# Kernel tuning notes

Hardware: AMD Instinct MI355X
Metric: run time of the kernel (lower is better)

The kernel has to match this reference:

```python
import jax, jax.numpy as jnp
import numpy as np

B, C, N, H = 2, 512, 3072, 8
D = C // H  # head_dim = 64


def setup_inputs() -> dict:
    key = jax.random.key(0)
    ks = jax.random.split(key, 8)
    s = 1.0 / np.sqrt(C)
    x = jax.random.normal(ks[0], (B, C, N), dtype=jnp.float32)
    adj = jax.random.randint(ks[1], (N, N), 0, 2, dtype=jnp.int32)
    adj = adj.at[jnp.arange(N), jnp.arange(N)].set(1)  # self-loops avoid empty rows
    geo_bias = jax.random.normal(ks[2], (N, N), dtype=jnp.float32) * 0.02
    Wq = jax.random.normal(ks[3], (C, C), dtype=jnp.float32) * s
    Wk = jax.random.normal(ks[4], (C, C), dtype=jnp.float32) * s
    Wv = jax.random.normal(ks[5], (C, C), dtype=jnp.float32) * s
    Wo = jax.random.normal(ks[6], (C, C), dtype=jnp.float32) * s
    z = jnp.zeros((C,), dtype=jnp.float32)
    return {"x": x, "adjacency": adj, "geo_bias": geo_bias,
            "Wq": Wq, "bq": z, "Wk": Wk, "bk": z, "Wv": Wv, "bv": z,
            "Wo": Wo, "bo": z}


def reference(x, adjacency, geo_bias, Wq, bq, Wk, bk, Wv, bv, Wo, bo):
    b, c, n = x.shape
    h, d = H, c // H
    feats = jnp.swapaxes(x, 1, 2)  # [B, N, C]
    # projections (nn.Linear: y = x @ W^T + b)
    q = feats @ Wq.T + bq
    k = feats @ Wk.T + bk
    v = feats @ Wv.T + bv
    # [B, H, N, D]
    q = q.reshape(b, n, h, d).transpose(0, 2, 1, 3)
    k = k.reshape(b, n, h, d).transpose(0, 2, 1, 3)
    v = v.reshape(b, n, h, d).transpose(0, 2, 1, 3)
    scores = jnp.einsum('bhnd,bhmd->bhnm', q, k) / jnp.sqrt(jnp.float32(d))
    scores = scores + geo_bias[None, None]
    scores = jnp.where(adjacency[None, None] == 0, -jnp.inf, scores)
    weights = jax.nn.softmax(scores, axis=-1)
    attended = jnp.einsum('bhnm,bhmd->bhnd', weights, v)
    attended = attended.transpose(0, 2, 1, 3).reshape(b, n, c)
    out = attended @ Wo.T + bo
    return jnp.swapaxes(out, 1, 2)  # [B, C, N]
```

## Files before the change

### kernel.cpp

```cpp
#include <hip/hip_runtime.h>

constexpr int Bb = 2, Cc = 512, Nn = 3072, Hh = 8, Dd = 64;
constexpr int BN = Bb * Nn;
constexpr int NT = Nn / 64;
constexpr int NTI = Nn / 128;

typedef __bf16 bf16;
typedef __attribute__((ext_vector_type(8))) __bf16 bf16x8;
typedef __attribute__((ext_vector_type(4))) __bf16 bf16x4;
typedef __attribute__((ext_vector_type(4))) float f32x4;
typedef __attribute__((ext_vector_type(16))) float f32x16;
typedef unsigned int u32;
typedef __attribute__((ext_vector_type(4))) u32 u32x4;

#define DEVINL static __device__ __forceinline__

DEVINL bf16x8 ldb8(const bf16* p) { return *reinterpret_cast<const bf16x8*>(p); }

DEVINL void gload_lds16(const bf16* g, bf16* l) {
    __builtin_amdgcn_global_load_lds(
        (const __attribute__((address_space(1))) void*)g,
        (__attribute__((address_space(3))) void*)l, 16, 0, 0);
}

DEVINL u32 cvtpk(float lo, float hi) {
    u32 r;
    asm("v_cvt_pk_bf16_f32 %0, %1, %2" : "=v"(r) : "v"(lo), "v"(hi));
    return r;
}
DEVINL void plswap(u32& a, u32& b) {
    asm("v_permlane32_swap_b32 %0, %1" : "+v"(a), "+v"(b));
}
DEVINL float xpair_sum(float v) { return v + __shfl_xor(v, 32); }

__global__ void k_tx(const float* __restrict__ x, bf16* __restrict__ feats) {
    __shared__ float t[32][33];
    const int b = blockIdx.z;
    const int n0 = blockIdx.x * 32, c0 = blockIdx.y * 32;
    const int tx = threadIdx.x, ty = threadIdx.y;
#pragma unroll
    for (int i = 0; i < 4; ++i)
        t[ty + i * 8][tx] = x[((size_t)b * Cc + c0 + ty + i * 8) * Nn + n0 + tx];
    __syncthreads();
#pragma unroll
    for (int i = 0; i < 4; ++i)
        feats[((size_t)b * Nn + n0 + ty + i * 8) * Cc + c0 + tx] = (bf16)t[tx][ty + i * 8];
}

__global__ void k_packw(const float* __restrict__ Wq, const float* __restrict__ Wk,
                        const float* __restrict__ Wv, const float* __restrict__ Wo,
                        bf16* __restrict__ Wqkv, bf16* __restrict__ WoB) {
    const int i = blockIdx.x * 256 + threadIdx.x;
    Wqkv[i]              = (bf16)Wq[i];
    Wqkv[i + 262144]     = (bf16)Wk[i];
    Wqkv[i + 524288]     = (bf16)Wv[i];
    WoB[i]               = (bf16)Wo[i];
}

__global__ void k_biasm(const int* __restrict__ adj, const float* __restrict__ gb,
                        bf16* __restrict__ biasF) {
    const int ti = blockIdx.x, tj = blockIdx.y;
    bf16* outp = biasF + ((size_t)ti * NT + tj) * 8192;
#pragma unroll
    for (int it = 0; it < 32; ++it) {
        const int p = it * 256 + threadIdx.x;
        const int w = p >> 11, hi = (p >> 10) & 1, l31 = (p >> 5) & 31;
        const int kt2 = (p >> 4) & 1, reg = p & 15;
        const int row = w * 32 + l31;
        const int col = kt2 * 32 + (reg & 3) + 8 * (reg >> 2) + 4 * hi;
        const size_t src = (size_t)(ti * 128 + row) * Nn + tj * 64 + col;
        outp[p] = adj[src] ? (bf16)(gb[src] * 1.44269504f) : (bf16)(-1e30f);
    }
}

#define STAGEG(dst, srcbase, ldk, k0, bi)                                      \
    {                                                                          \
        _Pragma("unroll")                                                      \
        for (int ps = 0; ps < 2; ++ps) {                                       \
            const int s = ps * 256 + tid;                                      \
            const int pr = s >> 3, pcb = s & 7;                                \
            const int cb = pcb ^ (pr & 7);                                     \
            gload_lds16((srcbase) + (size_t)pr * (ldk) + (k0) + cb * 8,        \
                        &dst[bi][(ps * 4 + w) * 512]);                         \
        }                                                                      \
    }

__global__ __launch_bounds__(256) void k_qkv(
        const bf16* __restrict__ feats, const bf16* __restrict__ Wqkv,
        const float* __restrict__ bq, const float* __restrict__ bk, const float* __restrict__ bv,
        bf16* __restrict__ Q, bf16* __restrict__ K, bf16* __restrict__ Vt) {
    __shared__ bf16 sA[2][4096];
    __shared__ bf16 sB[2][4096];
    const int m0 = blockIdx.x * 64;
    const int n0 = blockIdx.y * 64;
    const int tid = threadIdx.x, w = tid >> 6, lane = tid & 63;
    const int lg = lane >> 4, lc = lane & 15;

    f32x4 acc[4];
    const f32x4 z4 = {0.f, 0.f, 0.f, 0.f};
#pragma unroll
    for (int jt = 0; jt < 4; ++jt) acc[jt] = z4;

    const bf16* Abase = feats + (size_t)m0 * Cc;
    const bf16* Bbase = Wqkv + (size_t)n0 * Cc;

    int buf = 0;
    STAGEG(sA, Abase, Cc, 0, 0);
    STAGEG(sB, Bbase, Cc, 0, 0);
    for (int kk = 0; kk < 8; ++kk) {
        const int kn = (kk + 1 < 8) ? kk + 1 : 7;
        STAGEG(sA, Abase, Cc, kn * 64, buf ^ 1);
        STAGEG(sB, Bbase, Cc, kn * 64, buf ^ 1);
        asm volatile("s_waitcnt vmcnt(4)" ::: "memory");
        __builtin_amdgcn_s_barrier();
        const int ra = w * 16 + lc;
#pragma unroll
        for (int ks = 0; ks < 2; ++ks) {
            bf16x8 a = ldb8(&sA[buf][ra * 64 + (((ks * 4 + lg) ^ (ra & 7)) * 8)]);
#pragma unroll
            for (int jt = 0; jt < 4; ++jt) {
                const int rb = jt * 16 + lc;
                bf16x8 bfr = ldb8(&sB[buf][rb * 64 + (((ks * 4 + lg) ^ (rb & 7)) * 8)]);
                acc[jt] = __builtin_amdgcn_mfma_f32_16x16x32_bf16(a, bfr, acc[jt], 0, 0, 0);
            }
        }
        __builtin_amdgcn_s_barrier();
        buf ^= 1;
    }
    asm volatile("s_waitcnt vmcnt(0)" ::: "memory");

    const int proj = n0 >> 9;
    const int head = (n0 >> 6) & 7;
    const float* bias = proj == 0 ? bq : (proj == 1 ? bk : bv);
#pragma unroll
    for (int jt = 0; jt < 4; ++jt) {
        const int dcol = jt * 16 + lc;
        const float bs = bias[(n0 & 511) + dcol];
#pragma unroll
        for (int r = 0; r < 4; ++r) {
            const int m = m0 + w * 16 + lg * 4 + r;
            const int b = m / Nn;
            const int n = m - b * Nn;
            const float v = acc[jt][r] + bs;
            if (proj == 0)
                Q[(((size_t)b * Hh + head) * Nn + n) * Dd + dcol] = (bf16)v;
            else if (proj == 1)
                K[(((size_t)b * Hh + head) * Nn + n) * Dd + dcol] = (bf16)v;
            else
                Vt[(((size_t)b * Hh + head) * Dd + dcol) * Nn + n] = (bf16)v;
        }
    }
}

template <bool DIRECT, int TCNT>
__global__ __launch_bounds__(256) void k_attn(
        const bf16* __restrict__ Q, const bf16* __restrict__ K, const bf16* __restrict__ Vt,
        const bf16* __restrict__ biasF, bf16* __restrict__ att,
        float* __restrict__ pO, float* __restrict__ pL) {
    __shared__ bf16 sK[2][4096];
    __shared__ bf16 sV[2][4096];

    const int ti = blockIdx.x;
    const int i0 = ti * 128;
    const int bh = blockIdx.y;
    const int b = bh >> 3, h = bh & 7;
    const int sp = blockIdx.z;
    const int t0 = sp * TCNT;
    const int tid = threadIdx.x, w = tid >> 6, lane = tid & 63;
    const int l31 = lane & 31, hi = lane >> 5;

    const bf16* Qb = Q  + (size_t)bh * Nn * Dd;
    const bf16* Kb = K  + (size_t)bh * Nn * Dd;
    const bf16* Vb = Vt + (size_t)bh * Dd * Nn;
    const bf16* bp = biasF + (size_t)ti * NT * 8192 + (size_t)(w * 64 + lane) * 32;

    bf16x8 aq[4];
    {
        const bf16* qp = Qb + (size_t)(i0 + w * 32 + l31) * Dd + hi * 8;
#pragma unroll
        for (int dm = 0; dm < 4; ++dm) aq[dm] = ldb8(qp + dm * 16);
    }

    f32x16 acc[2];
#pragma unroll
    for (int dm = 0; dm < 2; ++dm)
#pragma unroll
        for (int i = 0; i < 16; ++i) acc[dm][i] = 0.f;
    float l16[16];
#pragma unroll
    for (int i = 0; i < 16; ++i) l16[i] = 0.f;

    constexpr float cqk = 0.18033688011112042f;

#define STAGE(bi, j0)                                                          \
    {                                                                          \
        _Pragma("unroll")                                                      \
        for (int u = 0; u < 2; ++u) {                                          \
            const int s = u * 256 + tid;                                       \
            const int pr = s >> 3, pcb = s & 7;                                \
            const int cb = pcb ^ (pr & 7);                                     \
            gload_lds16(Kb + (size_t)((j0) + pr) * Dd + cb * 8,                \
                        &sK[bi][(u * 4 + w) * 512]);                           \
            gload_lds16(Vb + (size_t)pr * Nn + (j0) + cb * 8,                  \
                        &sV[bi][(u * 4 + w) * 512]);                           \
        }                                                                      \
    }

    int buf = 0;
    STAGE(0, t0 * 64);
    bf16x8 bcur[4];
#pragma unroll
    for (int f = 0; f < 4; ++f) bcur[f] = ldb8(bp + (size_t)t0 * 8192 + f * 8);

    for (int u0 = 0; u0 < TCNT; ++u0) {
        const int tj = t0 + u0;
        const int tjn = (u0 + 1 < TCNT) ? tj + 1 : tj;
        STAGE(buf ^ 1, tjn * 64);
        bf16x8 bnx[4];
#pragma unroll
        for (int f = 0; f < 4; ++f) bnx[f] = ldb8(bp + (size_t)tjn * 8192 + f * 8);

        asm volatile("s_waitcnt vmcnt(8)" ::: "memory");
        __builtin_amdgcn_s_barrier();

        f32x16 s0, s1;
#pragma unroll
        for (int i = 0; i < 16; ++i) { s0[i] = 0.f; s1[i] = 0.f; }
        __builtin_amdgcn_s_setprio(1);
#pragma unroll
        for (int dm = 0; dm < 4; ++dm) {
            const int r0 = l31;
            bf16x8 kf0 = ldb8(&sK[buf][r0 * 64 + (((dm * 2 + hi) ^ (r0 & 7)) * 8)]);
            s0 = __builtin_amdgcn_mfma_f32_32x32x16_bf16(kf0, aq[dm], s0, 0, 0, 0);
            const int r1 = 32 + l31;
            bf16x8 kf1 = ldb8(&sK[buf][r1 * 64 + (((dm * 2 + hi) ^ (r1 & 7)) * 8)]);
            s1 = __builtin_amdgcn_mfma_f32_32x32x16_bf16(kf1, aq[dm], s1, 0, 0, 0);
        }
        __builtin_amdgcn_s_setprio(0);

        float sv[32];
#pragma unroll
        for (int i = 0; i < 16; ++i)
            sv[i] = __builtin_amdgcn_exp2f(__builtin_fmaf(s0[i], cqk, (float)bcur[i >> 3][i & 7]));
#pragma unroll
        for (int i = 0; i < 16; ++i)
            sv[16 + i] = __builtin_amdgcn_exp2f(__builtin_fmaf(s1[i], cqk, (float)bcur[2 + (i >> 3)][i & 7]));

#pragma unroll
        for (int i = 0; i < 16; ++i) l16[i] += sv[i] + sv[i + 16];

        bf16x8 pf[4];
#pragma unroll
        for (int g = 0; g < 4; ++g) {
            u32 X0 = cvtpk(sv[g * 8 + 0], sv[g * 8 + 1]);
            u32 X1 = cvtpk(sv[g * 8 + 2], sv[g * 8 + 3]);
            u32 Y0 = cvtpk(sv[g * 8 + 4], sv[g * 8 + 5]);
            u32 Y1 = cvtpk(sv[g * 8 + 6], sv[g * 8 + 7]);
            plswap(X0, Y0);
            plswap(X1, Y1);
            u32x4 t4 = {X0, X1, Y0, Y1};
            pf[g] = __builtin_bit_cast(bf16x8, t4);
        }

        __builtin_amdgcn_s_setprio(1);
#pragma unroll
        for (int dm = 0; dm < 2; ++dm)
#pragma unroll
            for (int kt = 0; kt < 4; ++kt) {
                const int rv = dm * 32 + l31;
                bf16x8 vf = ldb8(&sV[buf][rv * 64 + (((kt * 2 + hi) ^ (rv & 7)) * 8)]);
                acc[dm] = __builtin_amdgcn_mfma_f32_32x32x16_bf16(vf, pf[kt], acc[dm], 0, 0, 0);
            }
        __builtin_amdgcn_s_setprio(0);

        __builtin_amdgcn_s_barrier();
#pragma unroll
        for (int f = 0; f < 4; ++f) bcur[f] = bnx[f];
        buf ^= 1;
    }
    asm volatile("s_waitcnt vmcnt(0)" ::: "memory");

#pragma unroll
    for (int i = 0; i < 8; ++i) l16[i] += l16[i + 8];
#pragma unroll
    for (int i = 0; i < 4; ++i) l16[i] += l16[i + 4];
    float lrow = (l16[0] + l16[1]) + (l16[2] + l16[3]);
    lrow = xpair_sum(lrow);

    const int q = i0 + w * 32 + l31;
    if (DIRECT) {
        const float inv = 1.f / lrow;
        bf16* ap = att + ((size_t)b * Nn + q) * Cc + h * 64;
#pragma unroll
        for (int dm = 0; dm < 2; ++dm)
#pragma unroll
            for (int rg = 0; rg < 4; ++rg) {
                bf16x4 o;
#pragma unroll
                for (int i = 0; i < 4; ++i) o[i] = (bf16)(acc[dm][rg * 4 + i] * inv);
                *reinterpret_cast<bf16x4*>(ap + dm * 32 + rg * 8 + hi * 4) = o;
            }
    } else {
        float* op = pO + ((size_t)(sp * Bb * Hh + bh) * Nn + q) * Dd;
#pragma unroll
        for (int dm = 0; dm < 2; ++dm)
#pragma unroll
            for (int rg = 0; rg < 4; ++rg) {
                f32x4 o;
#pragma unroll
                for (int i = 0; i < 4; ++i) o[i] = acc[dm][rg * 4 + i];
                *reinterpret_cast<f32x4*>(op + dm * 32 + rg * 8 + hi * 4) = o;
            }
        if (hi == 0) pL[(size_t)(sp * Bb * Hh + bh) * Nn + q] = lrow;
    }
#undef STAGE
}

__global__ __launch_bounds__(256) void k_comb(const float* __restrict__ pO,
                                              const float* __restrict__ pL,
                                              bf16* __restrict__ att, int nsplit) {
    const int bh = blockIdx.y, b = bh >> 3, h = bh & 7;
    const int q = blockIdx.x * 64 + (threadIdx.x >> 2);
    const int d0 = (threadIdx.x & 3) * 16;
    const size_t base = ((size_t)bh * Nn + q) * Dd + d0;
    const size_t soff = (size_t)Bb * Hh * Nn * Dd;
    const size_t loff = (size_t)Bb * Hh * Nn;
    float l = 0.f;
    f32x4 o[4];
#pragma unroll
    for (int i = 0; i < 4; ++i) o[i] = f32x4{0.f, 0.f, 0.f, 0.f};
    for (int s = 0; s < nsplit; ++s) {
        l += pL[s * loff + (size_t)bh * Nn + q];
#pragma unroll
        for (int i = 0; i < 4; ++i) {
            f32x4 o2 = *reinterpret_cast<const f32x4*>(pO + s * soff + base + i * 4);
#pragma unroll
            for (int j = 0; j < 4; ++j) o[i][j] += o2[j];
        }
    }
    const float inv = 1.f / l;
    bf16* ap = att + ((size_t)b * Nn + q) * Cc + h * 64 + d0;
#pragma unroll
    for (int i = 0; i < 4; ++i) {
        bf16x4 ov;
#pragma unroll
        for (int j = 0; j < 4; ++j) ov[j] = (bf16)(o[i][j] * inv);
        *reinterpret_cast<bf16x4*>(ap + i * 4) = ov;
    }
}

__global__ __launch_bounds__(256) void k_out(
        const bf16* __restrict__ att, const bf16* __restrict__ WoB,
        const float* __restrict__ bo, float* __restrict__ out) {
    __shared__ bf16 sA[2][4096];
    __shared__ bf16 sB[2][4096];
    const int m0 = blockIdx.x * 64;
    const int n0 = blockIdx.y * 64;
    const int tid = threadIdx.x, w = tid >> 6, lane = tid & 63;
    const int lg = lane >> 4, lc = lane & 15;

    f32x4 acc[4];
    const f32x4 z4 = {0.f, 0.f, 0.f, 0.f};
#pragma unroll
    for (int jt = 0; jt < 4; ++jt) acc[jt] = z4;

    const bf16* Abase = att + (size_t)m0 * Cc;
    const bf16* Bbase = WoB + (size_t)n0 * Cc;

    int buf = 0;
    STAGEG(sA, Abase, Cc, 0, 0);
    STAGEG(sB, Bbase, Cc, 0, 0);
    for (int kk = 0; kk < 8; ++kk) {
        const int kn = (kk + 1 < 8) ? kk + 1 : 7;
        STAGEG(sA, Abase, Cc, kn * 64, buf ^ 1);
        STAGEG(sB, Bbase, Cc, kn * 64, buf ^ 1);
        asm volatile("s_waitcnt vmcnt(4)" ::: "memory");
        __builtin_amdgcn_s_barrier();
        const int ra = w * 16 + lc;
#pragma unroll
        for (int ks = 0; ks < 2; ++ks) {
            bf16x8 a = ldb8(&sA[buf][ra * 64 + (((ks * 4 + lg) ^ (ra & 7)) * 8)]);
#pragma unroll
            for (int jt = 0; jt < 4; ++jt) {
                const int rb = jt * 16 + lc;
                bf16x8 bfr = ldb8(&sB[buf][rb * 64 + (((ks * 4 + lg) ^ (rb & 7)) * 8)]);
                acc[jt] = __builtin_amdgcn_mfma_f32_16x16x32_bf16(a, bfr, acc[jt], 0, 0, 0);
            }
        }
        __builtin_amdgcn_s_barrier();
        buf ^= 1;
    }
    asm volatile("s_waitcnt vmcnt(0)" ::: "memory");

    const int m = m0 + w * 16 + lg * 4;
    const int b = m / Nn;
    const int n = m - b * Nn;
#pragma unroll
    for (int jt = 0; jt < 4; ++jt) {
        const int col = n0 + jt * 16 + lc;
        const float bs = bo[col];
        f32x4 vv;
#pragma unroll
        for (int r = 0; r < 4; ++r) vv[r] = acc[jt][r] + bs;
        *reinterpret_cast<f32x4*>(&out[((size_t)b * Cc + col) * Nn + n]) = vv;
    }
}

extern "C" void kernel_launch(void* const* d_in, const int* in_sizes, int n_in,
                              void* d_out, int out_size, void* d_ws, size_t ws_size,
                              hipStream_t stream) {
    (void)in_sizes; (void)n_in; (void)out_size;
    const float* x  = (const float*)d_in[0];
    const int*   adj= (const int*)d_in[1];
    const float* gb = (const float*)d_in[2];
    const float* Wq = (const float*)d_in[3];
    const float* bq = (const float*)d_in[4];
    const float* Wk = (const float*)d_in[5];
    const float* bk = (const float*)d_in[6];
    const float* Wv = (const float*)d_in[7];
    const float* bv = (const float*)d_in[8];
    const float* Wo = (const float*)d_in[9];
    const float* bo = (const float*)d_in[10];
    float* out = (float*)d_out;

    char* ws = (char*)d_ws;
    bf16*  feats = (bf16*)(ws);
    bf16*  Wqkv  = (bf16*)(ws + 6291456);
    bf16*  WoB   = (bf16*)(ws + 7864320);
    bf16*  Qm    = (bf16*)(ws + 8388608);
    bf16*  Km    = (bf16*)(ws + 14680064);
    bf16*  Vt    = (bf16*)(ws + 20971520);
    bf16*  att   = (bf16*)(ws + 27262976);
    bf16*  biasF = (bf16*)(ws + 33554432);
    float* pO    = (float*)(ws + 52428800);

    const size_t PO1 = 12582912ull, PL1 = 196608ull, BASE = 52428800ull;
    const size_t need4 = BASE + 4 * PO1 + 4 * PL1;
    const size_t need2 = BASE + 2 * PO1 + 2 * PL1;
    const size_t need1 = BASE + 1 * PO1 + 1 * PL1;

    k_tx   <<<dim3(Nn / 32, Cc / 32, Bb), dim3(32, 8), 0, stream>>>(x, feats);
    k_packw<<<dim3(1024), dim3(256), 0, stream>>>(Wq, Wk, Wv, Wo, Wqkv, WoB);
    k_biasm<<<dim3(NTI, NT), dim3(256), 0, stream>>>(adj, gb, biasF);
    k_qkv  <<<dim3(BN / 64, 1536 / 64), dim3(256), 0, stream>>>(feats, Wqkv, bq, bk, bv, Qm, Km, Vt);

    if (ws_size >= need4) {
        float* pL = (float*)(ws + BASE + 4 * PO1);
        k_attn<false, NT / 4><<<dim3(NTI, Bb * Hh, 4), dim3(256), 0, stream>>>(
            Qm, Km, Vt, biasF, att, pO, pL);
        k_comb<<<dim3(Nn / 64, Bb * Hh), dim3(256), 0, stream>>>(pO, pL, att, 4);
    } else if (ws_size >= need2) {
        float* pL = (float*)(ws + BASE + 2 * PO1);
        k_attn<false, NT / 2><<<dim3(NTI, Bb * Hh, 2), dim3(256), 0, stream>>>(
            Qm, Km, Vt, biasF, att, pO, pL);
        k_comb<<<dim3(Nn / 64, Bb * Hh), dim3(256), 0, stream>>>(pO, pL, att, 2);
    } else if (ws_size >= need1) {
        float* pL = (float*)(ws + BASE + 1 * PO1);
        k_attn<false, NT><<<dim3(NTI, Bb * Hh, 1), dim3(256), 0, stream>>>(
            Qm, Km, Vt, biasF, att, pO, pL);
        k_comb<<<dim3(Nn / 64, Bb * Hh), dim3(256), 0, stream>>>(pO, pL, att, 1);
    } else {
        k_attn<true, NT><<<dim3(NTI, Bb * Hh, 1), dim3(256), 0, stream>>>(
            Qm, Km, Vt, biasF, att, pO, (float*)pO);
    }
    k_out  <<<dim3(BN / 64, Cc / 64), dim3(256), 0, stream>>>(att, WoB, bo, out);
}
```

Measured before the change: 156.9 us.

## Enlarge projection GEMM tiles to 128x128 and drop 4-way attention split

The QKV and output projection GEMMs move from 64x64 to 128x128 block tiles, with each wave computing a 64x64 sub-tile of 4x4 MFMA fragments so every loaded A and B fragment is reused across more MFMAs. This cuts LDS and global traffic per FLOP but uses more registers and LDS, and launches fewer blocks (for example 48x4=192 blocks for k_out). Separately, the 4-way key-split attention path is removed, so attention now uses the 2-way split with a combine step, trading partial-sum traffic against parallelism.

```diff
diff --git a/kernel.cpp b/kernel.cpp
--- a/kernel.cpp
+++ b/kernel.cpp
@@ -73,15 +73,37 @@
     }
 }
 
-#define STAGEG(dst, srcbase, ldk, k0, bi)                                      \
+#define STAGE128(dst, srcbase, ldk, k0, bi)                                    \
     {                                                                          \
         _Pragma("unroll")                                                      \
-        for (int ps = 0; ps < 2; ++ps) {                                       \
-            const int s = ps * 256 + tid;                                      \
+        for (int uu = 0; uu < 4; ++uu) {                                       \
+            const int s = uu * 256 + tid;                                      \
             const int pr = s >> 3, pcb = s & 7;                                \
             const int cb = pcb ^ (pr & 7);                                     \
             gload_lds16((srcbase) + (size_t)pr * (ldk) + (k0) + cb * 8,        \
-                        &dst[bi][(ps * 4 + w) * 512]);                         \
+                        &dst[bi][(uu * 4 + w) * 512]);                         \
+        }                                                                      \
+    }
+
+#define GEMM128_STEP(bi)                                                       \
+    {                                                                          \
+        _Pragma("unroll")                                                      \
+        for (int ks = 0; ks < 2; ++ks) {                                       \
+            bf16x8 af[4];                                                      \
+            _Pragma("unroll")                                                  \
+            for (int rt = 0; rt < 4; ++rt) {                                   \
+                const int ra = wr * 64 + rt * 16 + lc;                         \
+                af[rt] = ldb8(&sA[bi][ra * 64 + (((ks * 4 + lg) ^ (ra & 7)) * 8)]); \
+            }                                                                  \
+            _Pragma("unroll")                                                  \
+            for (int ct = 0; ct < 4; ++ct) {                                   \
+                const int rb = wc * 64 + ct * 16 + lc;                         \
+                bf16x8 bfv = ldb8(&sB[bi][rb * 64 + (((ks * 4 + lg) ^ (rb & 7)) * 8)]); \
+                _Pragma("unroll")                                              \
+                for (int rt = 0; rt < 4; ++rt)                                 \
+                    acc[rt][ct] = __builtin_amdgcn_mfma_f32_16x16x32_bf16(     \
+                        af[rt], bfv, acc[rt][ct], 0, 0, 0);                    \
+            }                                                                  \
         }                                                                      \
     }
 
@@ -89,65 +111,61 @@
         const bf16* __restrict__ feats, const bf16* __restrict__ Wqkv,
         const float* __restrict__ bq, const float* __restrict__ bk, const float* __restrict__ bv,
         bf16* __restrict__ Q, bf16* __restrict__ K, bf16* __restrict__ Vt) {
-    __shared__ bf16 sA[2][4096];
-    __shared__ bf16 sB[2][4096];
-    const int m0 = blockIdx.x * 64;
-    const int n0 = blockIdx.y * 64;
+    __shared__ bf16 sA[2][8192];
+    __shared__ bf16 sB[2][8192];
+    const int m0 = blockIdx.x * 128;
+    const int n0 = blockIdx.y * 128;
     const int tid = threadIdx.x, w = tid >> 6, lane = tid & 63;
     const int lg = lane >> 4, lc = lane & 15;
-
-    f32x4 acc[4];
+    const int wr = w >> 1, wc = w & 1;
+
+    f32x4 acc[4][4];
     const f32x4 z4 = {0.f, 0.f, 0.f, 0.f};
 #pragma unroll
-    for (int jt = 0; jt < 4; ++jt) acc[jt] = z4;
+    for (int rt = 0; rt < 4; ++rt)
+#pragma unroll
+        for (int ct = 0; ct < 4; ++ct) acc[rt][ct] = z4;
 
     const bf16* Abase = feats + (size_t)m0 * Cc;
     const bf16* Bbase = Wqkv + (size_t)n0 * Cc;
 
     int buf = 0;
-    STAGEG(sA, Abase, Cc, 0, 0);
-    STAGEG(sB, Bbase, Cc, 0, 0);
+    STAGE128(sA, Abase, Cc, 0, 0);
+    STAGE128(sB, Bbase, Cc, 0, 0);
     for (int kk = 0; kk < 8; ++kk) {
         const int kn = (kk + 1 < 8) ? kk + 1 : 7;
-        STAGEG(sA, Abase, Cc, kn * 64, buf ^ 1);
-        STAGEG(sB, Bbase, Cc, kn * 64, buf ^ 1);
-        asm volatile("s_waitcnt vmcnt(4)" ::: "memory");
-        __builtin_amdgcn_s_barrier();
-        const int ra = w * 16 + lc;
-#pragma unroll
-        for (int ks = 0; ks < 2; ++ks) {
-            bf16x8 a = ldb8(&sA[buf][ra * 64 + (((ks * 4 + lg) ^ (ra & 7)) * 8)]);
-#pragma unroll
-            for (int jt = 0; jt < 4; ++jt) {
-                const int rb = jt * 16 + lc;
-                bf16x8 bfr = ldb8(&sB[buf][rb * 64 + (((ks * 4 + lg) ^ (rb & 7)) * 8)]);
-                acc[jt] = __builtin_amdgcn_mfma_f32_16x16x32_bf16(a, bfr, acc[jt], 0, 0, 0);
+        STAGE128(sA, Abase, Cc, kn * 64, buf ^ 1);
+        STAGE128(sB, Bbase, Cc, kn * 64, buf ^ 1);
+        asm volatile("s_waitcnt vmcnt(8)" ::: "memory");
+        __builtin_amdgcn_s_barrier();
+        GEMM128_STEP(buf);
+        __builtin_amdgcn_s_barrier();
+        buf ^= 1;
+    }
+    asm volatile("s_waitcnt vmcnt(0)" ::: "memory");
+
+    const int proj = n0 >> 9;
+    const int head = ((n0 & 511) >> 6) + wc;
+    const float* bias = proj == 0 ? bq : (proj == 1 ? bk : bv);
+#pragma unroll
+    for (int ct = 0; ct < 4; ++ct) {
+        const int d = ct * 16 + lc;
+        const float bs = bias[(n0 & 511) + wc * 64 + d];
+#pragma unroll
+        for (int rt = 0; rt < 4; ++rt) {
+#pragma unroll
+            for (int i = 0; i < 4; ++i) {
+                const int m = m0 + wr * 64 + rt * 16 + lg * 4 + i;
+                const int b = m / Nn;
+                const int n = m - b * Nn;
+                const float v = acc[rt][ct][i] + bs;
+                if (proj == 0)
+                    Q[(((size_t)b * Hh + head) * Nn + n) * Dd + d] = (bf16)v;
+                else if (proj == 1)
+                    K[(((size_t)b * Hh + head) * Nn + n) * Dd + d] = (bf16)v;
+                else
+                    Vt[(((size_t)b * Hh + head) * Dd + d) * Nn + n] = (bf16)v;
             }
-        }
-        __builtin_amdgcn_s_barrier();
-        buf ^= 1;
-    }
-    asm volatile("s_waitcnt vmcnt(0)" ::: "memory");
-
-    const int proj = n0 >> 9;
-    const int head = (n0 >> 6) & 7;
-    const float* bias = proj == 0 ? bq : (proj == 1 ? bk : bv);
-#pragma unroll
-    for (int jt = 0; jt < 4; ++jt) {
-        const int dcol = jt * 16 + lc;
-        const float bs = bias[(n0 & 511) + dcol];
-#pragma unroll
-        for (int r = 0; r < 4; ++r) {
-            const int m = m0 + w * 16 + lg * 4 + r;
-            const int b = m / Nn;
-            const int n = m - b * Nn;
-            const float v = acc[jt][r] + bs;
-            if (proj == 0)
-                Q[(((size_t)b * Hh + head) * Nn + n) * Dd + dcol] = (bf16)v;
-            else if (proj == 1)
-                K[(((size_t)b * Hh + head) * Nn + n) * Dd + dcol] = (bf16)v;
-            else
-                Vt[(((size_t)b * Hh + head) * Dd + dcol) * Nn + n] = (bf16)v;
         }
     }
 }
@@ -352,57 +370,53 @@
 __global__ __launch_bounds__(256) void k_out(
         const bf16* __restrict__ att, const bf16* __restrict__ WoB,
         const float* __restrict__ bo, float* __restrict__ out) {
-    __shared__ bf16 sA[2][4096];
-    __shared__ bf16 sB[2][4096];
-    const int m0 = blockIdx.x * 64;
-    const int n0 = blockIdx.y * 64;
+    __shared__ bf16 sA[2][8192];
+    __shared__ bf16 sB[2][8192];
+    const int m0 = blockIdx.x * 128;
+    const int n0 = blockIdx.y * 128;
     const int tid = threadIdx.x, w = tid >> 6, lane = tid & 63;
     const int lg = lane >> 4, lc = lane & 15;
-
-    f32x4 acc[4];
+    const int wr = w >> 1, wc = w & 1;
+
+    f32x4 acc[4][4];
     const f32x4 z4 = {0.f, 0.f, 0.f, 0.f};
 #pragma unroll
-    for (int jt = 0; jt < 4; ++jt) acc[jt] = z4;
+    for (int rt = 0; rt < 4; ++rt)
+#pragma unroll
+        for (int ct = 0; ct < 4; ++ct) acc[rt][ct] = z4;
 
     const bf16* Abase = att + (size_t)m0 * Cc;
     const bf16* Bbase = WoB + (size_t)n0 * Cc;
 
     int buf = 0;
-    STAGEG(sA, Abase, Cc, 0, 0);
-    STAGEG(sB, Bbase, Cc, 0, 0);
+    STAGE128(sA, Abase, Cc, 0, 0);
+    STAGE128(sB, Bbase, Cc, 0, 0);
     for (int kk = 0; kk < 8; ++kk) {
         const int kn = (kk + 1 < 8) ? kk + 1 : 7;
-        STAGEG(sA, Abase, Cc, kn * 64, buf ^ 1);
-        STAGEG(sB, Bbase, Cc, kn * 64, buf ^ 1);
-        asm volatile("s_waitcnt vmcnt(4)" ::: "memory");
-        __builtin_amdgcn_s_barrier();
-        const int ra = w * 16 + lc;
-#pragma unroll
-        for (int ks = 0; ks < 2; ++ks) {
-            bf16x8 a = ldb8(&sA[buf][ra * 64 + (((ks * 4 + lg) ^ (ra & 7)) * 8)]);
-#pragma unroll
-            for (int jt = 0; jt < 4; ++jt) {
-                const int rb = jt * 16 + lc;
-                bf16x8 bfr = ldb8(&sB[buf][rb * 64 + (((ks * 4 + lg) ^ (rb & 7)) * 8)]);
-                acc[jt] = __builtin_amdgcn_mfma_f32_16x16x32_bf16(a, bfr, acc[jt], 0, 0, 0);
-            }
+        STAGE128(sA, Abase, Cc, kn * 64, buf ^ 1);
+        STAGE128(sB, Bbase, Cc, kn * 64, buf ^ 1);
+        asm volatile("s_waitcnt vmcnt(8)" ::: "memory");
+        __builtin_amdgcn_s_barrier();
+        GEMM128_STEP(buf);
+        __builtin_amdgcn_s_barrier();
+        buf ^= 1;
+    }
+    asm volatile("s_waitcnt vmcnt(0)" ::: "memory");
+
+#pragma unroll
+    for (int ct = 0; ct < 4; ++ct) {
+        const int col = n0 + wc * 64 + ct * 16 + lc;
+        const float bs = bo[col];
+#pragma unroll
+        for (int rt = 0; rt < 4; ++rt) {
+            const int m = m0 + wr * 64 + rt * 16 + lg * 4;
+            const int b = m / Nn;
+            const int n = m - b * Nn;
+            f32x4 vv;
+#pragma unroll
+            for (int i = 0; i < 4; ++i) vv[i] = acc[rt][ct][i] + bs;
+            *reinterpret_cast<f32x4*>(&out[((size_t)b * Cc + col) * Nn + n]) = vv;
         }
-        __builtin_amdgcn_s_barrier();
-        buf ^= 1;
-    }
-    asm volatile("s_waitcnt vmcnt(0)" ::: "memory");
-
-    const int m = m0 + w * 16 + lg * 4;
-    const int b = m / Nn;
-    const int n = m - b * Nn;
-#pragma unroll
-    for (int jt = 0; jt < 4; ++jt) {
-        const int col = n0 + jt * 16 + lc;
-        const float bs = bo[col];
-        f32x4 vv;
-#pragma unroll
-        for (int r = 0; r < 4; ++r) vv[r] = acc[jt][r] + bs;
-        *reinterpret_cast<f32x4*>(&out[((size_t)b * Cc + col) * Nn + n]) = vv;
     }
 }
 
@@ -435,21 +449,15 @@
     float* pO    = (float*)(ws + 52428800);
 
     const size_t PO1 = 12582912ull, PL1 = 196608ull, BASE = 52428800ull;
-    const size_t need4 = BASE + 4 * PO1 + 4 * PL1;
     const size_t need2 = BASE + 2 * PO1 + 2 * PL1;
     const size_t need1 = BASE + 1 * PO1 + 1 * PL1;
 
     k_tx   <<<dim3(Nn / 32, Cc / 32, Bb), dim3(32, 8), 0, stream>>>(x, feats);
     k_packw<<<dim3(1024), dim3(256), 0, stream>>>(Wq, Wk, Wv, Wo, Wqkv, WoB);
     k_biasm<<<dim3(NTI, NT), dim3(256), 0, stream>>>(adj, gb, biasF);
-    k_qkv  <<<dim3(BN / 64, 1536 / 64), dim3(256), 0, stream>>>(feats, Wqkv, bq, bk, bv, Qm, Km, Vt);
-
-    if (ws_size >= need4) {
-        float* pL = (float*)(ws + BASE + 4 * PO1);
-        k_attn<false, NT / 4><<<dim3(NTI, Bb * Hh, 4), dim3(256), 0, stream>>>(
-            Qm, Km, Vt, biasF, att, pO, pL);
-        k_comb<<<dim3(Nn / 64, Bb * Hh), dim3(256), 0, stream>>>(pO, pL, att, 4);
-    } else if (ws_size >= need2) {
+    k_qkv  <<<dim3(BN / 128, 1536 / 128), dim3(256), 0, stream>>>(feats, Wqkv, bq, bk, bv, Qm, Km, Vt);
+
+    if (ws_size >= need2) {
         float* pL = (float*)(ws + BASE + 2 * PO1);
         k_attn<false, NT / 2><<<dim3(NTI, Bb * Hh, 2), dim3(256), 0, stream>>>(
             Qm, Km, Vt, biasF, att, pO, pL);
@@ -463,5 +471,5 @@
         k_attn<true, NT><<<dim3(NTI, Bb * Hh, 1), dim3(256), 0, stream>>>(
             Qm, Km, Vt, biasF, att, pO, (float*)pO);
     }
-    k_out  <<<dim3(BN / 64, Cc / 64), dim3(256), 0, stream>>>(att, WoB, bo, out);
-}
+    k_out  <<<dim3(BN / 128, Cc / 128), dim3(256), 0, stream>>>(att, WoB, bo, out);
+}
```

Measured after the change: 162.9 us. 1.04x slower.
